# Performance work log

Measured on AMD Instinct MI355X. Metric: run time of the kernel, lower is better.

The kernel has to match this reference:

```python
import jax, jax.numpy as jnp
import numpy as np

B, T, C, K, V = 4, 2048, 1024, 1024, 1024
SQRT_K = float(np.sqrt(K))


def setup_inputs() -> dict:
    key = jax.random.key(0)
    ks = jax.random.split(key, 7)
    s = 0.02
    return {
        "x": jax.random.normal(ks[0], (B, T, C), jnp.float32),
        "Wq": (jax.random.normal(ks[1], (C, K), jnp.float32) * s),
        "bq": jnp.zeros((K,), jnp.float32),
        "Wk": (jax.random.normal(ks[2], (C, K), jnp.float32) * s),
        "bk": jnp.zeros((K,), jnp.float32),
        "Wv": (jax.random.normal(ks[3], (C, V), jnp.float32) * s),
        "bv": jnp.zeros((V,), jnp.float32),
    }


def reference(x, Wq, bq, Wk, bk, Wv, bv):
    # projections: [B,T,C] @ [C,K] -> [B,T,K]
    q = x @ Wq + bq
    k = x @ Wk + bk
    v = x @ Wv + bv
    # logits[b,t,s] = q[b,t,:] . k[b,s,:]
    logits = jnp.einsum("btk,bsk->bts", q, k)
    # original mask: mask[j,i] = 1 if i > j -> strict upper triangle masked to -inf
    seq = logits.shape[1]
    mask = jnp.triu(jnp.ones((seq, seq), bool), k=1)
    logits = jnp.where(mask[None, :, :], -jnp.inf, logits)
    # NOTE: original softmax is over dim=1 (query axis), not the key axis
    probs = jax.nn.softmax(logits / SQRT_K, axis=1)
    read = jnp.einsum("bts,bsv->btv", probs, v)
    return jnp.concatenate((x, read), axis=2)
```

## Files before the change

### kernel.cpp

```cpp
#include <hip/hip_runtime.h>
#include <hip/hip_bf16.h>
#include <stdint.h>

#define DEVI __device__ __forceinline__

using u16 = unsigned short;
typedef __attribute__((ext_vector_type(8))) _Float16 halfx8;
typedef __attribute__((ext_vector_type(8))) unsigned short u16x8;
typedef __attribute__((ext_vector_type(4))) float f32x4;

constexpr int BB = 4, TT = 2048, CC = 1024, KD = 1024, VD = 1024;
constexpr int QKVW = 3072;
constexpr int OUTW = CC + VD;
constexpr float INV_SQRT_K = 0.03125f;

DEVI u16 f2h(float f) {
  _Float16 h = (_Float16)f;
  return __builtin_bit_cast(u16, h);
}
DEVI float h2f(u16 u) {
  return (float)__builtin_bit_cast(_Float16, u);
}

DEVI void gload16(const u16* g, u16* l) {
  __builtin_amdgcn_global_load_lds(
      (const __attribute__((address_space(1))) void*)g,
      (__attribute__((address_space(3))) void*)l, 16, 0, 0);
}

__global__ void cast_x_copy(const float* __restrict__ x, u16* __restrict__ xh,
                            float* __restrict__ out) {
  size_t i = (size_t)blockIdx.x * blockDim.x + threadIdx.x;
  float4 v = reinterpret_cast<const float4*>(x)[i];
  ushort4 u;
  u.x = f2h(v.x); u.y = f2h(v.y); u.z = f2h(v.z); u.w = f2h(v.w);
  reinterpret_cast<ushort4*>(xh)[i] = u;
  size_t e = i * 4;
  size_t bt = e / CC;
  int c = (int)(e % CC);
  *reinterpret_cast<float4*>(&out[bt * OUTW + c]) = v;
}

__global__ void transpose_cast_w(const float* __restrict__ W, u16* __restrict__ Wt) {
  __shared__ float tile[32][33];
  int n0 = blockIdx.x * 32, c0 = blockIdx.y * 32;
  int tx = threadIdx.x, ty = threadIdx.y;
  for (int i = ty; i < 32; i += 8)
    tile[i][tx] = W[(size_t)(c0 + i) * KD + n0 + tx];
  __syncthreads();
  for (int i = ty; i < 32; i += 8)
    Wt[(size_t)(n0 + i) * CC + c0 + tx] = f2h(tile[tx][i]);
}

__global__ void concat_bias(const float* __restrict__ bq, const float* __restrict__ bk,
                            const float* __restrict__ bv, float* __restrict__ bc) {
  int n = blockIdx.x * 256 + threadIdx.x;
  float v = (n < 1024) ? bq[n] : (n < 2048) ? bk[n - 1024] : bv[n - 2048];
  bc[n] = v;
}

__global__ void transpose_v(const u16* __restrict__ QKV, u16* __restrict__ Vt) {
  __shared__ u16 tile[32][33];
  int b = blockIdx.z;
  int n0 = blockIdx.x * 32, s0 = blockIdx.y * 32;
  const u16* src = QKV + (size_t)b * TT * QKVW + 2048;
  u16* dst = Vt + (size_t)b * VD * TT;
  int tx = threadIdx.x, ty = threadIdx.y;
  for (int i = ty; i < 32; i += 8)
    tile[i][tx] = src[(size_t)(s0 + i) * QKVW + n0 + tx];
  __syncthreads();
  for (int i = ty; i < 32; i += 8)
    dst[(size_t)(n0 + i) * TT + s0 + tx] = tile[tx][i];
}

template <typename OutT, int SWZ, bool CSKIP, bool KLIM, bool BIAS, bool CMASK>
__global__ __launch_bounds__(512, 2) void gemm_bt(
    const u16* __restrict__ A, const u16* __restrict__ Bm, OutT* __restrict__ Out,
    const float* __restrict__ bias, float* __restrict__ Dp,
    int Kd, int lda, int ldb, int ldo,
    long long strA, long long strB, long long strO, float alpha) {
  constexpr int BM = 256, BN = 128, BK = 32;
  constexpr int WM = 4, WN = 2;
  constexpr int WR = 64, WC = 64;
  constexpr int MR = 4, NR = 4;
  constexpr int ASZ = BM * BK, BSZ = BN * BK;
  __shared__ u16 sA[3 * ASZ];
  __shared__ u16 sB[3 * BSZ];
  __shared__ float reds[CMASK ? WM : 1][CMASK ? BN : 1];

  int bx = blockIdx.x, by = blockIdx.y;
  if constexpr (SWZ == 1) {
    const int gx = gridDim.x;
    const int nx = gx >> 3;
    int fid = bx + gx * by;
    int xcd = fid & 7, idx = fid >> 3;
    bx = xcd * nx + idx % nx;
    by = idx / nx;
  }
  const int r0 = bx * BM, c0 = by * BN;
  if (CSKIP && c0 > r0 + BM - 1) return;
  A   += (size_t)blockIdx.z * strA;
  Bm  += (size_t)blockIdx.z * strB;
  Out += (size_t)blockIdx.z * strO;

  const int tid = threadIdx.x;
  const int lane = tid & 63;
  const int w = tid >> 6;
  const int wm = w / WN, wn = w % WN;
  const int l15 = lane & 15, l4 = lane >> 4;
  const int cswz8 = 8 * (l4 ^ ((l15 >> 1) & 3));

  const int srow = tid >> 2;
  const int sc8 = 8 * ((tid & 3) ^ ((tid >> 3) & 3));
  const u16* gA  = A  + (size_t)(r0 + srow) * lda + sc8;
  const u16* gA2 = gA + (size_t)128 * lda;
  const u16* gB  = Bm + (size_t)(c0 + srow) * ldb + sc8;
  const int sdst = tid * 8;

  f32x4 acc[MR][NR] = {};

  int kmax = Kd;
  if (KLIM) { int km = r0 + BM; kmax = km < Kd ? km : Kd; }
  const int NT = kmax / BK;

  auto stage = [&](int buf, int kt) {
    const int k0 = kt * BK;
    u16* da = sA + buf * ASZ + sdst;
    gload16(gA + k0, da);
    gload16(gA2 + k0, da + 4096);
    u16* db = sB + buf * BSZ + sdst;
    gload16(gB + k0, db);
  };

  stage(0, 0);
  stage(1, 1);
  asm volatile("s_waitcnt vmcnt(3)" ::: "memory");
  __builtin_amdgcn_s_barrier();

  int buf = 0;
  for (int kt = 0; kt < NT; ++kt) {
    int nb = buf + 2; if (nb >= 3) nb -= 3;
    const u16* rA = sA + buf * ASZ;
    const u16* rB = sB + buf * BSZ;
    halfx8 af[MR], bfv[NR];
#pragma unroll
    for (int n = 0; n < NR; ++n)
      bfv[n] = *reinterpret_cast<const halfx8*>(&rB[(wn * WC + n * 16 + l15) * BK + cswz8]);
#pragma unroll
    for (int m = 0; m < MR; ++m)
      af[m] = *reinterpret_cast<const halfx8*>(&rA[(wm * WR + m * 16 + l15) * BK + cswz8]);
    if (kt + 2 < NT) stage(nb, kt + 2);
    __builtin_amdgcn_s_setprio(1);
#pragma unroll
    for (int m = 0; m < MR; ++m)
#pragma unroll
      for (int n = 0; n < NR; ++n)
        acc[m][n] = __builtin_amdgcn_mfma_f32_16x16x32_f16(af[m], bfv[n], acc[m][n], 0, 0, 0);
    __builtin_amdgcn_s_setprio(0);
    if (kt + 2 < NT)      asm volatile("s_waitcnt vmcnt(3)" ::: "memory");
    else if (kt + 1 < NT) asm volatile("s_waitcnt vmcnt(0)" ::: "memory");
    if (kt + 1 < NT) __builtin_amdgcn_s_barrier();
    buf = buf + 1; if (buf == 3) buf = 0;
  }

  if constexpr (CMASK) {
#pragma unroll
    for (int n = 0; n < NR; ++n) {
      const int gcol = c0 + wn * WC + n * 16 + l15;
      float sm = 0.f;
#pragma unroll
      for (int m = 0; m < MR; ++m) {
        const int growb = r0 + wm * WR + m * 16 + l4 * 4;
#pragma unroll
        for (int r = 0; r < 4; ++r) {
          float p = 0.f;
          if (growb + r >= gcol) p = __expf(acc[m][n][r] * alpha);
          reinterpret_cast<u16*>(Out)[(size_t)(growb + r) * ldo + gcol] = f2h(p);
          sm += p;
        }
      }
      sm += __shfl_xor(sm, 16);
      sm += __shfl_xor(sm, 32);
      if (l4 == 0) reds[wm][wn * WC + n * 16 + l15] = sm;
    }
    __syncthreads();
    if (tid < BN) {
      float d2 = 0.f;
#pragma unroll
      for (int i = 0; i < WM; ++i) d2 += reds[i][tid];
      Dp[((size_t)(r0 >> 8) * BB + blockIdx.z) * TT + c0 + tid] = d2;
    }
  } else {
#pragma unroll
    for (int m = 0; m < MR; ++m) {
      const int growb = r0 + wm * WR + m * 16 + l4 * 4;
#pragma unroll
      for (int n = 0; n < NR; ++n) {
        const int gcol = c0 + wn * WC + n * 16 + l15;
        float bvv = 0.f;
        if (BIAS) bvv = bias[gcol];
#pragma unroll
        for (int r = 0; r < 4; ++r) {
          float val = acc[m][n][r] * alpha + bvv;
          size_t off = (size_t)(growb + r) * ldo + gcol;
          if constexpr (sizeof(OutT) == 2) {
            reinterpret_cast<u16*>(Out)[off] = f2h(val);
          } else {
            reinterpret_cast<float*>(Out)[off] = val;
          }
        }
      }
    }
  }
}

__global__ void stats_combine(const float* __restrict__ Dp, float* __restrict__ Di) {
  int b = blockIdx.y;
  int s = blockIdx.x * 256 + threadIdx.x;
  int rt0 = s >> 8;
  float d = 0.f;
  for (int rt = rt0; rt < TT / 256; ++rt)
    d += Dp[((size_t)rt * BB + b) * TT + s];
  Di[b * TT + s] = 1.f / d;
}

__global__ void scale_vt(u16* __restrict__ Vt, const float* __restrict__ Di) {
  size_t i = ((size_t)blockIdx.x * 256 + threadIdx.x) * 8;
  int b = (int)(i >> 21);
  int s = (int)(i & (TT - 1));
  u16x8 v = *reinterpret_cast<u16x8*>(&Vt[i]);
  const float* Db = Di + b * TT + s;
#pragma unroll
  for (int j = 0; j < 8; ++j) v[j] = f2h(h2f(v[j]) * Db[j]);
  *reinterpret_cast<u16x8*>(&Vt[i]) = v;
}

extern "C" void kernel_launch(void* const* d_in, const int* in_sizes, int n_in,
                              void* d_out, int out_size, void* d_ws, size_t ws_size,
                              hipStream_t stream) {
  const float* x  = (const float*)d_in[0];
  const float* Wq = (const float*)d_in[1];
  const float* bq = (const float*)d_in[2];
  const float* Wk = (const float*)d_in[3];
  const float* bk = (const float*)d_in[4];
  const float* Wv = (const float*)d_in[5];
  const float* bv = (const float*)d_in[6];
  float* out = (float*)d_out;
  char* ws = (char*)d_ws;
  constexpr size_t MB = 1024ull * 1024ull;

  u16* xh   = (u16*)(ws);
  u16* QKV  = (u16*)(ws + 16 * MB);
  u16* Wt   = (u16*)(ws + 64 * MB);
  float* bc = (float*)(ws + 70 * MB);
  u16* SP   = (u16*)(ws + 71 * MB);
  u16* Vt = xh;
  float* Dp = (float*)(ws + 64 * MB);
  float* Di = (float*)(ws + 65 * MB);

  cast_x_copy<<<dim3((BB * TT * CC / 4) / 256), dim3(256), 0, stream>>>(x, xh, out);
  dim3 tb(32, 8);
  transpose_cast_w<<<dim3(KD / 32, CC / 32), tb, 0, stream>>>(Wq, Wt);
  transpose_cast_w<<<dim3(KD / 32, CC / 32), tb, 0, stream>>>(Wk, Wt + 1024 * 1024);
  transpose_cast_w<<<dim3(VD / 32, CC / 32), tb, 0, stream>>>(Wv, Wt + 2048 * 1024);
  concat_bias<<<dim3(QKVW / 256), 256, 0, stream>>>(bq, bk, bv, bc);

  gemm_bt<u16, 1, false, false, true, false><<<dim3(32, QKVW / 128, 1), 512, 0, stream>>>(
      xh, Wt, QKV, bc, nullptr, CC, CC, CC, QKVW, 0, 0, 0, 1.f);

  transpose_v<<<dim3(VD / 32, TT / 32, BB), tb, 0, stream>>>(QKV, Vt);

  gemm_bt<u16, 0, true, false, false, true><<<dim3(TT / 256, TT / 128, BB), 512, 0, stream>>>(
      QKV, QKV + 1024, SP, nullptr, Dp, KD, QKVW, QKVW, TT,
      (long long)TT * QKVW, (long long)TT * QKVW, (long long)TT * TT, INV_SQRT_K);

  stats_combine<<<dim3(TT / 256, BB), 256, 0, stream>>>(Dp, Di);
  scale_vt<<<dim3(BB * VD * TT / 8 / 256), 256, 0, stream>>>(Vt, Di);

  gemm_bt<float, 0, false, true, false, false><<<dim3(TT / 256, VD / 128, BB), 512, 0, stream>>>(
      SP, Vt, out + CC, nullptr, nullptr, TT, TT, TT, OUTW,
      (long long)TT * TT, (long long)VD * TT, (long long)TT * OUTW, 1.f);
}
```

Before: 194.1 us.

## Fuse V scaling into transpose, merge weight transposes, switch GEMM to double buffering

Moves the V transpose after the softmax statistics so it applies the per-key reciprocal sum while transposing, which removes the separate scale_vt pass over Vt. The three weight transpose launches become one launch over a z-dimension of 3. Separately, the GEMM pipeline drops from a three-stage to a two-stage LDS buffer with a full vmcnt(0) wait each iteration. That cuts shared memory per block but gives up one stage of prefetch latency hiding.

```diff
diff --git a/kernel.cpp b/kernel.cpp
--- a/kernel.cpp
+++ b/kernel.cpp
@@ -41,15 +41,20 @@
   *reinterpret_cast<float4*>(&out[bt * OUTW + c]) = v;
 }
 
-__global__ void transpose_cast_w(const float* __restrict__ W, u16* __restrict__ Wt) {
+__global__ void transpose_cast_w3(const float* __restrict__ Wq,
+                                  const float* __restrict__ Wk,
+                                  const float* __restrict__ Wv,
+                                  u16* __restrict__ Wt) {
   __shared__ float tile[32][33];
+  const float* W = (blockIdx.z == 0) ? Wq : (blockIdx.z == 1) ? Wk : Wv;
+  u16* dst = Wt + (size_t)blockIdx.z * 1024 * 1024;
   int n0 = blockIdx.x * 32, c0 = blockIdx.y * 32;
   int tx = threadIdx.x, ty = threadIdx.y;
   for (int i = ty; i < 32; i += 8)
     tile[i][tx] = W[(size_t)(c0 + i) * KD + n0 + tx];
   __syncthreads();
   for (int i = ty; i < 32; i += 8)
-    Wt[(size_t)(n0 + i) * CC + c0 + tx] = f2h(tile[tx][i]);
+    dst[(size_t)(n0 + i) * CC + c0 + tx] = f2h(tile[tx][i]);
 }
 
 __global__ void concat_bias(const float* __restrict__ bq, const float* __restrict__ bk,
@@ -59,7 +64,8 @@
   bc[n] = v;
 }
 
-__global__ void transpose_v(const u16* __restrict__ QKV, u16* __restrict__ Vt) {
+__global__ void transpose_v(const u16* __restrict__ QKV, const float* __restrict__ Di,
+                            u16* __restrict__ Vt) {
   __shared__ u16 tile[32][33];
   int b = blockIdx.z;
   int n0 = blockIdx.x * 32, s0 = blockIdx.y * 32;
@@ -68,9 +74,10 @@
   int tx = threadIdx.x, ty = threadIdx.y;
   for (int i = ty; i < 32; i += 8)
     tile[i][tx] = src[(size_t)(s0 + i) * QKVW + n0 + tx];
+  float di = Di[b * TT + s0 + tx];
   __syncthreads();
   for (int i = ty; i < 32; i += 8)
-    dst[(size_t)(n0 + i) * TT + s0 + tx] = tile[tx][i];
+    dst[(size_t)(n0 + i) * TT + s0 + tx] = f2h(h2f(tile[tx][i]) * di);
 }
 
 template <typename OutT, int SWZ, bool CSKIP, bool KLIM, bool BIAS, bool CMASK>
@@ -84,8 +91,8 @@
   constexpr int WR = 64, WC = 64;
   constexpr int MR = 4, NR = 4;
   constexpr int ASZ = BM * BK, BSZ = BN * BK;
-  __shared__ u16 sA[3 * ASZ];
-  __shared__ u16 sB[3 * BSZ];
+  __shared__ u16 sA[2 * ASZ];
+  __shared__ u16 sB[2 * BSZ];
   __shared__ float reds[CMASK ? WM : 1][CMASK ? BN : 1];
 
   int bx = blockIdx.x, by = blockIdx.y;
@@ -133,13 +140,12 @@
   };
 
   stage(0, 0);
-  stage(1, 1);
-  asm volatile("s_waitcnt vmcnt(3)" ::: "memory");
+  asm volatile("s_waitcnt vmcnt(0)" ::: "memory");
   __builtin_amdgcn_s_barrier();
 
-  int buf = 0;
   for (int kt = 0; kt < NT; ++kt) {
-    int nb = buf + 2; if (nb >= 3) nb -= 3;
+    const int buf = kt & 1;
+    if (kt + 1 < NT) stage(buf ^ 1, kt + 1);
     const u16* rA = sA + buf * ASZ;
     const u16* rB = sB + buf * BSZ;
     halfx8 af[MR], bfv[NR];
@@ -149,7 +155,6 @@
 #pragma unroll
     for (int m = 0; m < MR; ++m)
       af[m] = *reinterpret_cast<const halfx8*>(&rA[(wm * WR + m * 16 + l15) * BK + cswz8]);
-    if (kt + 2 < NT) stage(nb, kt + 2);
     __builtin_amdgcn_s_setprio(1);
 #pragma unroll
     for (int m = 0; m < MR; ++m)
@@ -157,10 +162,10 @@
       for (int n = 0; n < NR; ++n)
         acc[m][n] = __builtin_amdgcn_mfma_f32_16x16x32_f16(af[m], bfv[n], acc[m][n], 0, 0, 0);
     __builtin_amdgcn_s_setprio(0);
-    if (kt + 2 < NT)      asm volatile("s_waitcnt vmcnt(3)" ::: "memory");
-    else if (kt + 1 < NT) asm volatile("s_waitcnt vmcnt(0)" ::: "memory");
-    if (kt + 1 < NT) __builtin_amdgcn_s_barrier();
-    buf = buf + 1; if (buf == 3) buf = 0;
+    if (kt + 1 < NT) {
+      asm volatile("s_waitcnt vmcnt(0)" ::: "memory");
+      __builtin_amdgcn_s_barrier();
+    }
   }
 
   if constexpr (CMASK) {
@@ -222,17 +227,6 @@
   for (int rt = rt0; rt < TT / 256; ++rt)
     d += Dp[((size_t)rt * BB + b) * TT + s];
   Di[b * TT + s] = 1.f / d;
-}
-
-__global__ void scale_vt(u16* __restrict__ Vt, const float* __restrict__ Di) {
-  size_t i = ((size_t)blockIdx.x * 256 + threadIdx.x) * 8;
-  int b = (int)(i >> 21);
-  int s = (int)(i & (TT - 1));
-  u16x8 v = *reinterpret_cast<u16x8*>(&Vt[i]);
-  const float* Db = Di + b * TT + s;
-#pragma unroll
-  for (int j = 0; j < 8; ++j) v[j] = f2h(h2f(v[j]) * Db[j]);
-  *reinterpret_cast<u16x8*>(&Vt[i]) = v;
 }
 
 extern "C" void kernel_launch(void* const* d_in, const int* in_sizes, int n_in,
@@ -260,22 +254,19 @@
 
   cast_x_copy<<<dim3((BB * TT * CC / 4) / 256), dim3(256), 0, stream>>>(x, xh, out);
   dim3 tb(32, 8);
-  transpose_cast_w<<<dim3(KD / 32, CC / 32), tb, 0, stream>>>(Wq, Wt);
-  transpose_cast_w<<<dim3(KD / 32, CC / 32), tb, 0, stream>>>(Wk, Wt + 1024 * 1024);
-  transpose_cast_w<<<dim3(VD / 32, CC / 32), tb, 0, stream>>>(Wv, Wt + 2048 * 1024);
+  transpose_cast_w3<<<dim3(KD / 32, CC / 32, 3), tb, 0, stream>>>(Wq, Wk, Wv, Wt);
   concat_bias<<<dim3(QKVW / 256), 256, 0, stream>>>(bq, bk, bv, bc);
 
   gemm_bt<u16, 1, false, false, true, false><<<dim3(32, QKVW / 128, 1), 512, 0, stream>>>(
       xh, Wt, QKV, bc, nullptr, CC, CC, CC, QKVW, 0, 0, 0, 1.f);
-
-  transpose_v<<<dim3(VD / 32, TT / 32, BB), tb, 0, stream>>>(QKV, Vt);
 
   gemm_bt<u16, 0, true, false, false, true><<<dim3(TT / 256, TT / 128, BB), 512, 0, stream>>>(
       QKV, QKV + 1024, SP, nullptr, Dp, KD, QKVW, QKVW, TT,
       (long long)TT * QKVW, (long long)TT * QKVW, (long long)TT * TT, INV_SQRT_K);
 
   stats_combine<<<dim3(TT / 256, BB), 256, 0, stream>>>(Dp, Di);
-  scale_vt<<<dim3(BB * VD * TT / 8 / 256), 256, 0, stream>>>(Vt, Di);
+
+  transpose_v<<<dim3(VD / 32, TT / 32, BB), tb, 0, stream>>>(QKV, Di, Vt);
 
   gemm_bt<float, 0, false, true, false, false><<<dim3(TT / 256, VD / 128, BB), 512, 0, stream>>>(
       SP, Vt, out + CC, nullptr, nullptr, TT, TT, TT, OUTW,
```

Result: slower. 203.6 us (+4.9%).
